# Kernel optimization log

Measured on AMD Instinct MI355X. Metric: run time of the kernel, lower is better.

The kernel has to match this reference:

```python
import jax, jax.numpy as jnp
import numpy as np

VOCAB = 50257
WORD_DIM = 300
HIDDEN = 256
BATCH = 256   # number of trees
LEAVES = 1024  # leaves per complete binary tree (power of 2)


def setup_inputs() -> dict:
    key = jax.random.key(0)
    k_ids, k_emb, k_w1, k_b1, k_w2, k_b2 = jax.random.split(key, 6)
    word_ids = jax.random.randint(k_ids, (BATCH, LEAVES), 0, VOCAB)
    emb_table = jax.random.normal(k_emb, (VOCAB, WORD_DIM), dtype=jnp.float32) * 0.1
    W1 = jax.random.normal(k_w1, (WORD_DIM, HIDDEN), dtype=jnp.float32) * (1.0 / np.sqrt(WORD_DIM))
    b1 = jax.random.normal(k_b1, (HIDDEN,), dtype=jnp.float32) * 0.01
    W2 = jax.random.normal(k_w2, (2 * HIDDEN, HIDDEN), dtype=jnp.float32) * (1.0 / np.sqrt(2 * HIDDEN))
    b2 = jax.random.normal(k_b2, (HIDDEN,), dtype=jnp.float32) * 0.01
    return {"word_ids": word_ids, "emb_table": emb_table, "W1": W1, "b1": b1, "W2": W2, "b2": b2}


def reference(word_ids, emb_table, W1, b1, W2, b2):
    # Leaves: embedding lookup + word2hidden linear (no nonlinearity, as in source)
    h = jnp.einsum('blw,wh->blh', emb_table[word_ids], W1) + b1  # [B, L, H]
    # Internal nodes: concat(left, right) @ W2 + b2, level by level up the
    # complete binary tree. Loop count = log2(LEAVES), a small static constant.
    while h.shape[1] > 1:
        B, n, H = h.shape
        pairs = h.reshape(B, n // 2, 2 * H)  # concat of sibling states
        h = jnp.einsum('bnk,kh->bnh', pairs, W2) + b2
    return h[:, 0, :]  # root hidden state per tree: [B, H]
```

## Files before the change

### kernel.cpp

```cpp
#include <hip/hip_runtime.h>
#include <hip/hip_bf16.h>
#include <stdint.h>

#define VOCAB 50257
#define WD 300
#define KP1 320
#define MP 50432

using bf16 = __hip_bfloat16;
typedef __attribute__((ext_vector_type(4))) float f32x4;
typedef __attribute__((ext_vector_type(8))) short bf16x8;

__device__ __forceinline__ void async_load16(const void* g, void* l) {
    __builtin_amdgcn_global_load_lds(
        (const __attribute__((address_space(1))) uint32_t*)(uintptr_t)g,
        (__attribute__((address_space(3))) uint32_t*)l, 16, 0, 0);
}

__global__ void prep_w(const float* __restrict__ W1, const float* __restrict__ W2,
                       const float* __restrict__ b2,
                       bf16* __restrict__ w1t, bf16* __restrict__ w2t,
                       bf16* __restrict__ w2b, float* __restrict__ b4,
                       float* __restrict__ zbuf) {
    if (blockIdx.x == 1344) {
        __shared__ float b2s[256];
        int n = threadIdx.x;
        b2s[n] = b2[n];
        zbuf[n] = 0.0f;
        __syncthreads();
        float acc = b2s[n];
        #pragma unroll 8
        for (int k = 0; k < 256; ++k)
            acc += b2s[k] * (W2[k * 256 + n] + W2[(k + 256) * 256 + n]);
        b4[n] = acc;
        return;
    }
    int idx = blockIdx.x * 256 + threadIdx.x;
    if (idx < 256 * KP1) {
        int n = idx / KP1;
        int k = idx - n * KP1;
        w1t[idx] = __float2bfloat16(k < WD ? W1[k * 256 + n] : 0.0f);
    } else if (idx < 256 * KP1 + 131072) {
        int j = idx - 256 * KP1;
        int n = j >> 9, k = j & 511;
        w2t[j] = __float2bfloat16(W2[k * 256 + n]);
    } else {
        int j = idx - 256 * KP1 - 131072;
        w2b[j] = __float2bfloat16(W2[j]);
    }
}

template <int AMODE, bool OUT_F32>
__device__ __forceinline__ void tile_gemm(
    char* smem, const void* Av, const int* ids,
    const bf16* BT, int Bstr, const float* bias,
    void* C, int Cs, int coff, int K, int As, int m0,
    const float* zbuf)
{
    constexpr int ASZ = (AMODE == 2) ? 16384 : 8192;
    constexpr int BSZ = 16384, STAGE = ASZ + BSZ;

    const int t = threadIdx.x, w = t >> 6, lane = t & 63;
    const int rg = w >> 2, cgr = w & 3, mi = lane & 15, q = lane >> 4;
    const bf16* Ab = (const bf16*)Av;

    auto stage = [&](int ke, int buf) {
        char* Asm = smem + buf * STAGE;
        char* Bsm = Asm + ASZ;
        if constexpr (AMODE == 2) {
            const float* A32 = (const float*)Av;
            #pragma unroll
            for (int i = 0; i < 2; ++i) {
                int s = i * 512 + t;
                int row = s >> 3;
                int kcd = (s & 7) ^ (row & 7);
                int k = ke + kcd * 4;
                int grow = m0 + row; if (grow >= VOCAB) grow = VOCAB - 1;
                const float* g = (k <= 296) ? (A32 + (size_t)grow * WD + k) : zbuf;
                async_load16(g, Asm + i * 8192 + w * 1024);
            }
        } else {
            int row = t >> 2;
            int kcd = (t & 3) ^ ((row >> 2) & 3);
            const bf16* g = Ab + (size_t)(m0 + row) * As + ke + kcd * 8;
            async_load16(g, Asm + w * 1024);
        }
        #pragma unroll
        for (int i = 0; i < 2; ++i) {
            int s = i * 512 + t;
            int col = s >> 2;
            int kcd = (s & 3) ^ ((col >> 2) & 3);
            async_load16(BT + (size_t)col * Bstr + ke + kcd * 8,
                         Bsm + i * 8192 + w * 1024);
        }
    };

    f32x4 acc[4][4] = {};

    auto compute = [&](int buf) {
        const char* Asm = smem + buf * STAGE;
        const bf16* Bs16 = (const bf16*)(Asm + ASZ);
        bf16x8 af[4], bfr[4];
        if constexpr (AMODE == 2) {
            const float* As32 = (const float*)Asm;
            #pragma unroll
            for (int r = 0; r < 4; ++r) {
                int row = rg * 64 + r * 16 + mi;
                int sl = row * 8 + ((2 * q) ^ (row & 7));
                f32x4 lo = *(const f32x4*)(As32 + sl * 4);
                f32x4 hi = *(const f32x4*)(As32 + (sl ^ 1) * 4);
                union { bf16x8 v; bf16 hh[8]; } u;
                #pragma unroll
                for (int j = 0; j < 4; ++j) u.hh[j] = __float2bfloat16(lo[j]);
                #pragma unroll
                for (int j = 0; j < 4; ++j) u.hh[4 + j] = __float2bfloat16(hi[j]);
                af[r] = u.v;
            }
        } else {
            const bf16* As16 = (const bf16*)Asm;
            #pragma unroll
            for (int r = 0; r < 4; ++r) {
                int row = rg * 64 + r * 16 + mi;
                int slot = row * 4 + (q ^ ((row >> 2) & 3));
                af[r] = *(const bf16x8*)(As16 + slot * 8);
            }
        }
        #pragma unroll
        for (int c = 0; c < 4; ++c) {
            int col = cgr * 64 + c * 16 + mi;
            int slot = col * 4 + (q ^ ((col >> 2) & 3));
            bfr[c] = *(const bf16x8*)(Bs16 + slot * 8);
        }
        #pragma unroll
        for (int r = 0; r < 4; ++r)
            #pragma unroll
            for (int c = 0; c < 4; ++c)
                acc[r][c] = __builtin_amdgcn_mfma_f32_16x16x32_bf16(af[r], bfr[c], acc[r][c], 0, 0, 0);
    };

    const int S = K >> 5;
    if constexpr (AMODE == 2) {
        stage(0, 0);
        for (int k0 = 0; k0 < S; ++k0) {
            if (k0 + 1 < S) {
                stage((k0 + 1) * 32, (k0 + 1) & 1);
                asm volatile("s_waitcnt vmcnt(4)\n\ts_barrier" ::: "memory");
            } else {
                asm volatile("s_waitcnt vmcnt(0)\n\ts_barrier" ::: "memory");
            }
            compute(k0 & 1);
            asm volatile("s_waitcnt lgkmcnt(0)\n\ts_barrier" ::: "memory");
        }
    } else {
        stage(0, 0);
        if (S > 1) stage(32, 1);
        for (int k0 = 0; k0 < S; ++k0) {
            if (k0 + 1 < S)
                asm volatile("s_waitcnt vmcnt(3)\n\ts_barrier" ::: "memory");
            else
                asm volatile("s_waitcnt vmcnt(0)\n\ts_barrier" ::: "memory");
            if (k0 + 2 < S) stage((k0 + 2) * 32, (k0 + 2) % 3);
            compute(k0 % 3);
        }
    }

    #pragma unroll
    for (int r = 0; r < 4; ++r) {
        int rowb = m0 + rg * 64 + r * 16 + q * 4;
        #pragma unroll
        for (int c = 0; c < 4; ++c) {
            int col = cgr * 64 + c * 16 + mi;
            float bv = bias[col];
            #pragma unroll
            for (int i = 0; i < 4; ++i) {
                float v = acc[r][c][i] + bv;
                size_t o = (size_t)(rowb + i) * Cs + coff + col;
                if (OUT_F32) ((float*)C)[o] = v;
                else         ((bf16*)C)[o] = __float2bfloat16(v);
            }
        }
    }
    (void)ids;
}

__global__ __launch_bounds__(512)
void combo(const float* __restrict__ emb, const bf16* __restrict__ w1t,
           const float* __restrict__ b1, const bf16* __restrict__ w2t,
           const bf16* __restrict__ w2b, bf16* __restrict__ w4t,
           bf16* __restrict__ proj, const float* __restrict__ zbuf) {
    __shared__ char smem[73728];
    int blk = blockIdx.x;
    if (blk < 8) {
        int j = blk >> 1, s = blk & 1;
        tile_gemm<0, false>(smem, w2t + 256 * (j >> 1), nullptr,
                            w2b + 65536 * (j & 1), 256, zbuf,
                            w4t, 1024, 256 * j, 256, 512, s * 128, nullptr);
    } else {
        tile_gemm<2, false>(smem, emb, nullptr, w1t, KP1, b1,
                            proj, 256, 0, KP1, WD, (blk - 8) * 128, zbuf);
    }
}

__global__ __launch_bounds__(512)
void w4cK(const bf16* __restrict__ w4t, bf16* __restrict__ w4c) {
    const int tid = blockIdx.x * 512 + threadIdx.x;
    #pragma unroll
    for (int i = 0; i < 8; ++i) {
        int u = i * 4096 + tid;
        int ln = u & 63, ks = (u >> 6) & 31, cg = u >> 11;
        int mi2 = ln & 15, q2 = ln >> 4;
        *(int4*)(w4c + (size_t)u * 8) =
            *(const int4*)(w4t + (size_t)(cg * 16 + mi2) * 1024 + ks * 32 + q2 * 8);
    }
}

__global__ __launch_bounds__(512)
void mainK(const bf16* __restrict__ proj, const int* __restrict__ ids,
           const bf16* __restrict__ w4c, const float* __restrict__ b4,
           bf16* __restrict__ h) {
    __shared__ char Abuf[4][8192];
    const int t = threadIdx.x, w = t >> 6, lane = t & 63;
    const int mi = lane & 15, q = lane >> 4;
    const int rt = blockIdx.x >> 1, ch = blockIdx.x & 1;
    const int m0 = rt * 128;
    const int c0 = ch * 128;
    const int cg = ch * 8 + w;

    const int4 idq = ((const int4*)ids)[m0 + (t >> 2)];

    auto stageA = [&](int r, int buf) {
        int ke = r * 32;
        int row = t >> 2;
        int kcd = (t & 3) ^ ((row >> 2) & 3);
        int sel = ke >> 8;
        int id = (sel & 2) ? ((sel & 1) ? idq.w : idq.z)
                           : ((sel & 1) ? idq.y : idq.x);
        async_load16(proj + (size_t)id * 256 + (ke & 255) + kcd * 8,
                     Abuf[buf] + w * 1024);
        (void)row;
    };

    f32x4 acc[8] = {};
    bf16x8 bp[2];

    stageA(0, 0); stageA(1, 1);
    bp[0] = *(const bf16x8*)(w4c + ((size_t)(cg * 32 + 0) * 64 + lane) * 8);

    #pragma unroll
    for (int r = 0; r < 32; ++r) {
        if (r + 2 < 32) stageA(r + 2, (r + 2) & 3);
        if (r + 1 < 32)
            bp[(r + 1) & 1] = *(const bf16x8*)(
                w4c + ((size_t)(cg * 32 + (r + 1)) * 64 + lane) * 8);
        if (r + 1 < 32)
            asm volatile("s_waitcnt vmcnt(2) lgkmcnt(0)\n\ts_barrier" ::: "memory");
        else
            asm volatile("s_waitcnt vmcnt(0) lgkmcnt(0)\n\ts_barrier" ::: "memory");
        const bf16* As16 = (const bf16*)Abuf[r & 3];
        #pragma unroll
        for (int ri = 0; ri < 8; ++ri) {
            int row = ri * 16 + mi;
            int slot = row * 4 + (q ^ ((row >> 2) & 3));
            bf16x8 af = *(const bf16x8*)(As16 + slot * 8);
            acc[ri] = __builtin_amdgcn_mfma_f32_16x16x32_bf16(af, bp[r & 1], acc[ri], 0, 0, 0);
        }
    }

    const int col = c0 + w * 16 + mi;
    const float bv = b4[col];
    #pragma unroll
    for (int ri = 0; ri < 8; ++ri) {
        int rowb = m0 + ri * 16 + q * 4;
        #pragma unroll
        for (int i = 0; i < 4; ++i)
            h[(size_t)(rowb + i) * 256 + col] = __float2bfloat16(acc[ri][i] + bv);
    }
}

__global__ __launch_bounds__(512)
void treeK(const bf16* __restrict__ h, const bf16* __restrict__ w4t,
           const bf16* __restrict__ w4c, const float* __restrict__ b4,
           float* __restrict__ out) {
    constexpr int ASZ = 8192, BSZ = 32768, STAGE = ASZ + BSZ;
    __shared__ char smem[2 * STAGE];
    __shared__ bf16 Ht[64 * 256];
    __shared__ bf16 Ht2[16 * 256];
    __shared__ bf16 Ht3[4 * 256];

    const int t = threadIdx.x, w = t >> 6, lane = t & 63;
    const int mi = lane & 15, q = lane >> 4;
    const int b = blockIdx.x;

    {
        auto stage = [&](int r, int buf) {
            char* As = smem + buf * STAGE;
            char* Bs = As + ASZ;
            const int kb = r * 64;
            {
                int row = t >> 3, c = t & 7;
                async_load16(h + (size_t)(64 * b + row) * 1024 + kb + ((c ^ (row & 7)) << 3),
                             As + w * 1024);
            }
            #pragma unroll
            for (int sub = 0; sub < 2; ++sub)
                #pragma unroll
                for (int i = 0; i < 2; ++i) {
                    int s = i * 512 + t;
                    int col = s >> 2;
                    int kcd = (s & 3) ^ ((col >> 2) & 3);
                    async_load16(w4t + (size_t)col * 1024 + kb + sub * 32 + kcd * 8,
                                 Bs + sub * 16384 + i * 8192 + w * 1024);
                }
        };
        f32x4 acc[4][2] = {};
        stage(0, 0);
        for (int r = 0; r < 16; ++r) {
            if (r + 1 < 16) {
                stage(r + 1, (r + 1) & 1);
                asm volatile("s_waitcnt vmcnt(5)\n\ts_barrier" ::: "memory");
            } else {
                asm volatile("s_waitcnt vmcnt(0)\n\ts_barrier" ::: "memory");
            }
            const bf16* As16 = (const bf16*)(smem + (r & 1) * STAGE);
            const bf16* Bb   = (const bf16*)(smem + (r & 1) * STAGE + ASZ);
            #pragma unroll
            for (int kk = 0; kk < 2; ++kk) {
                bf16x8 af[4], bfr[2];
                #pragma unroll
                for (int ri = 0; ri < 4; ++ri) {
                    int row = ri * 16 + mi;
                    int c = kk * 4 + q;
                    af[ri] = *(const bf16x8*)(As16 + (row * 8 + (c ^ (row & 7))) * 8);
                }
                #pragma unroll
                for (int c4 = 0; c4 < 2; ++c4) {
                    int col = w * 32 + c4 * 16 + mi;
                    int slot = col * 4 + (q ^ ((col >> 2) & 3));
                    bfr[c4] = *(const bf16x8*)(Bb + kk * 8192 + slot * 8);
                }
                #pragma unroll
                for (int ri = 0; ri < 4; ++ri)
                    #pragma unroll
                    for (int c4 = 0; c4 < 2; ++c4)
                        acc[ri][c4] = __builtin_amdgcn_mfma_f32_16x16x32_bf16(af[ri], bfr[c4], acc[ri][c4], 0, 0, 0);
            }
            asm volatile("s_waitcnt lgkmcnt(0)\n\ts_barrier" ::: "memory");
        }
        #pragma unroll
        for (int ri = 0; ri < 4; ++ri) {
            #pragma unroll
            for (int c4 = 0; c4 < 2; ++c4) {
                int col = w * 32 + c4 * 16 + mi;
                float bv = b4[col];
                int chunk = col >> 3;
                #pragma unroll
                for (int i = 0; i < 4; ++i) {
                    int row = ri * 16 + q * 4 + i;
                    Ht[(row * 32 + (chunk ^ (row & 31))) * 8 + (col & 7)] =
                        __float2bfloat16(acc[ri][c4][i] + bv);
                }
            }
        }
    }
    __syncthreads();

    {
        f32x4 acc[2] = {};
        #pragma unroll 8
        for (int ks = 0; ks < 32; ++ks) {
            int kc = (ks & 7) * 4 + q;
            int r2 = 4 * mi + (ks >> 3);
            bf16x8 a = *(const bf16x8*)(Ht + (r2 * 32 + (kc ^ (r2 & 31))) * 8);
            #pragma unroll
            for (int g = 0; g < 2; ++g) {
                bf16x8 bb = *(const bf16x8*)(w4c + ((size_t)((2 * w + g) * 32 + ks) * 64 + lane) * 8);
                acc[g] = __builtin_amdgcn_mfma_f32_16x16x32_bf16(a, bb, acc[g], 0, 0, 0);
            }
        }
        #pragma unroll
        for (int g = 0; g < 2; ++g) {
            int col = w * 32 + g * 16 + mi;
            float bv = b4[col];
            int chunk = col >> 3;
            #pragma unroll
            for (int i = 0; i < 4; ++i) {
                int row = q * 4 + i;
                Ht2[(row * 32 + (chunk ^ (row & 15))) * 8 + (col & 7)] =
                    __float2bfloat16(acc[g][i] + bv);
            }
        }
    }
    __syncthreads();

    {
        f32x4 acc[2] = {};
        #pragma unroll 8
        for (int ks = 0; ks < 32; ++ks) {
            int kc = (ks & 7) * 4 + q;
            int r3 = (4 * mi + (ks >> 3)) & 15;
            bf16x8 a = *(const bf16x8*)(Ht2 + (r3 * 32 + (kc ^ (r3 & 15))) * 8);
            #pragma unroll
            for (int g = 0; g < 2; ++g) {
                bf16x8 bb = *(const bf16x8*)(w4c + ((size_t)((2 * w + g) * 32 + ks) * 64 + lane) * 8);
                acc[g] = __builtin_amdgcn_mfma_f32_16x16x32_bf16(a, bb, acc[g], 0, 0, 0);
            }
        }
        if (q == 0) {
            #pragma unroll
            for (int g = 0; g < 2; ++g) {
                int col = w * 32 + g * 16 + mi;
                float bv = b4[col];
                #pragma unroll
                for (int i = 0; i < 4; ++i)
                    Ht3[i * 256 + col] = __float2bfloat16(acc[g][i] + bv);
            }
        }
    }
    __syncthreads();

    {
        f32x4 acc[2] = {};
        #pragma unroll 8
        for (int ks = 0; ks < 32; ++ks) {
            int r4 = (4 * mi + (ks >> 3)) & 3;
            bf16x8 a = *(const bf16x8*)(Ht3 + r4 * 256 + (ks & 7) * 32 + q * 8);
            #pragma unroll
            for (int g = 0; g < 2; ++g) {
                bf16x8 bb = *(const bf16x8*)(w4c + ((size_t)((2 * w + g) * 32 + ks) * 64 + lane) * 8);
                acc[g] = __builtin_amdgcn_mfma_f32_16x16x32_bf16(a, bb, acc[g], 0, 0, 0);
            }
        }
        if (q == 0) {
            #pragma unroll
            for (int g = 0; g < 2; ++g) {
                int col = w * 32 + g * 16 + mi;
                out[(size_t)b * 256 + col] = acc[g][0] + b4[col];
            }
        }
    }
}

extern "C" void kernel_launch(void* const* d_in, const int* in_sizes, int n_in,
                              void* d_out, int out_size, void* d_ws, size_t ws_size,
                              hipStream_t stream) {
    const int*   ids = (const int*)d_in[0];
    const float* emb = (const float*)d_in[1];
    const float* W1  = (const float*)d_in[2];
    const float* b1  = (const float*)d_in[3];
    const float* W2  = (const float*)d_in[4];
    const float* b2  = (const float*)d_in[5];
    (void)in_sizes; (void)n_in; (void)out_size; (void)ws_size;

    char* ws = (char*)d_ws;
    size_t off = 0;
    float* zbuf = (float*)(ws + off); off += 1024;
    float* b4   = (float*)(ws + off); off += 1024;
    bf16* w1t = (bf16*)(ws + off); off += (size_t)256 * KP1 * 2;
    bf16* w2t = (bf16*)(ws + off); off += (size_t)256 * 512 * 2;
    bf16* w2b = (bf16*)(ws + off); off += (size_t)512 * 256 * 2;
    bf16* w4t = (bf16*)(ws + off); off += (size_t)256 * 1024 * 2;
    bf16* w4c = (bf16*)(ws + off); off += (size_t)256 * 1024 * 2;
    bf16* proj = (bf16*)(ws + off); off += (size_t)MP * 256 * 2;
    bf16* h  = (bf16*)(ws + off); off += (size_t)65536 * 256 * 2;
    (void)off;

    prep_w<<<1345, 256, 0, stream>>>(W1, W2, b2, w1t, w2t, w2b, b4, zbuf);

    combo<<<402, 512, 0, stream>>>(emb, w1t, b1, w2t, w2b, w4t, proj, zbuf);

    w4cK<<<8, 512, 0, stream>>>(w4t, w4c);

    mainK<<<1024, 512, 0, stream>>>(proj, ids, w4c, b4, h);

    treeK<<<256, 512, 0, stream>>>(h, w4t, w4c, b4, (float*)d_out);
}
```

Baseline: 223.0 us.

## Compute full 256-column output per block with 4x4 register tiles in mainK

mainK now has each block cover all 256 output columns for its 128 rows instead of splitting columns across two blocks, which halves the grid to 512 blocks. Each wave computes a 64x64 tile (4 row fragments by 4 column fragments) so every A fragment read from LDS is reused across four B fragments, and the gathered A rows are loaded only once. The aim is to remove the duplicated A gathers and cut LDS reads per MFMA. In exchange it raises register pressure (16 accumulators plus 8 B fragments) and halves the number of blocks, with wait counts retuned for the larger B prefetch.

```diff
diff --git a/kernel.cpp b/kernel.cpp
--- a/kernel.cpp
+++ b/kernel.cpp
@@ -220,60 +220,83 @@
            bf16* __restrict__ h) {
     __shared__ char Abuf[4][8192];
     const int t = threadIdx.x, w = t >> 6, lane = t & 63;
-    const int mi = lane & 15, q = lane >> 4;
-    const int rt = blockIdx.x >> 1, ch = blockIdx.x & 1;
-    const int m0 = rt * 128;
-    const int c0 = ch * 128;
-    const int cg = ch * 8 + w;
+    const int rg = w >> 2, cgr = w & 3, mi = lane & 15, q = lane >> 4;
+    const int m0 = blockIdx.x * 128;
 
     const int4 idq = ((const int4*)ids)[m0 + (t >> 2)];
 
     auto stageA = [&](int r, int buf) {
         int ke = r * 32;
-        int row = t >> 2;
-        int kcd = (t & 3) ^ ((row >> 2) & 3);
+        int kcd = (t & 3) ^ (((t >> 2) >> 2) & 3);
         int sel = ke >> 8;
         int id = (sel & 2) ? ((sel & 1) ? idq.w : idq.z)
                            : ((sel & 1) ? idq.y : idq.x);
         async_load16(proj + (size_t)id * 256 + (ke & 255) + kcd * 8,
                      Abuf[buf] + w * 1024);
-        (void)row;
-    };
-
-    f32x4 acc[8] = {};
-    bf16x8 bp[2];
+    };
+
+    f32x4 acc[4][4] = {};
+    bf16x8 bp0[4], bp1[4];
+
+    auto loadB0 = [&](int r) {
+        #pragma unroll
+        for (int c = 0; c < 4; ++c)
+            bp0[c] = *(const bf16x8*)(
+                w4c + ((size_t)((cgr * 4 + c) * 32 + r) * 64 + lane) * 8);
+    };
+    auto loadB1 = [&](int r) {
+        #pragma unroll
+        for (int c = 0; c < 4; ++c)
+            bp1[c] = *(const bf16x8*)(
+                w4c + ((size_t)((cgr * 4 + c) * 32 + r) * 64 + lane) * 8);
+    };
+
+    auto doMfma = [&](const bf16* As16, const bf16x8* bp) {
+        bf16x8 af[4];
+        #pragma unroll
+        for (int ri = 0; ri < 4; ++ri) {
+            int row = rg * 64 + ri * 16 + mi;
+            int slot = row * 4 + (q ^ ((row >> 2) & 3));
+            af[ri] = *(const bf16x8*)(As16 + slot * 8);
+        }
+        #pragma unroll
+        for (int ri = 0; ri < 4; ++ri)
+            #pragma unroll
+            for (int c = 0; c < 4; ++c)
+                acc[ri][c] = __builtin_amdgcn_mfma_f32_16x16x32_bf16(
+                    af[ri], bp[c], acc[ri][c], 0, 0, 0);
+    };
 
     stageA(0, 0); stageA(1, 1);
-    bp[0] = *(const bf16x8*)(w4c + ((size_t)(cg * 32 + 0) * 64 + lane) * 8);
+    loadB0(0);
+
+    for (int rr = 0; rr < 30; rr += 2) {
+        stageA(rr + 2, (rr + 2) & 3);
+        loadB1(rr + 1);
+        asm volatile("s_waitcnt vmcnt(10) lgkmcnt(0)\n\ts_barrier" ::: "memory");
+        doMfma((const bf16*)Abuf[rr & 3], bp0);
+        stageA(rr + 3, (rr + 3) & 3);
+        loadB0(rr + 2);
+        asm volatile("s_waitcnt vmcnt(10) lgkmcnt(0)\n\ts_barrier" ::: "memory");
+        doMfma((const bf16*)Abuf[(rr + 1) & 3], bp1);
+    }
+    loadB1(31);
+    asm volatile("s_waitcnt vmcnt(9) lgkmcnt(0)\n\ts_barrier" ::: "memory");
+    doMfma((const bf16*)Abuf[30 & 3], bp0);
+    asm volatile("s_waitcnt vmcnt(0) lgkmcnt(0)\n\ts_barrier" ::: "memory");
+    doMfma((const bf16*)Abuf[31 & 3], bp1);
 
     #pragma unroll
-    for (int r = 0; r < 32; ++r) {
-        if (r + 2 < 32) stageA(r + 2, (r + 2) & 3);
-        if (r + 1 < 32)
-            bp[(r + 1) & 1] = *(const bf16x8*)(
-                w4c + ((size_t)(cg * 32 + (r + 1)) * 64 + lane) * 8);
-        if (r + 1 < 32)
-            asm volatile("s_waitcnt vmcnt(2) lgkmcnt(0)\n\ts_barrier" ::: "memory");
-        else
-            asm volatile("s_waitcnt vmcnt(0) lgkmcnt(0)\n\ts_barrier" ::: "memory");
-        const bf16* As16 = (const bf16*)Abuf[r & 3];
-        #pragma unroll
-        for (int ri = 0; ri < 8; ++ri) {
-            int row = ri * 16 + mi;
-            int slot = row * 4 + (q ^ ((row >> 2) & 3));
-            bf16x8 af = *(const bf16x8*)(As16 + slot * 8);
-            acc[ri] = __builtin_amdgcn_mfma_f32_16x16x32_bf16(af, bp[r & 1], acc[ri], 0, 0, 0);
-        }
-    }
-
-    const int col = c0 + w * 16 + mi;
-    const float bv = b4[col];
-    #pragma unroll
-    for (int ri = 0; ri < 8; ++ri) {
-        int rowb = m0 + ri * 16 + q * 4;
-        #pragma unroll
-        for (int i = 0; i < 4; ++i)
-            h[(size_t)(rowb + i) * 256 + col] = __float2bfloat16(acc[ri][i] + bv);
+    for (int ri = 0; ri < 4; ++ri) {
+        int rowb = m0 + rg * 64 + ri * 16 + q * 4;
+        #pragma unroll
+        for (int c = 0; c < 4; ++c) {
+            int col = cgr * 64 + c * 16 + mi;
+            float bv = b4[col];
+            #pragma unroll
+            for (int i = 0; i < 4; ++i)
+                h[(size_t)(rowb + i) * 256 + col] = __float2bfloat16(acc[ri][c][i] + bv);
+        }
     }
 }
 
@@ -470,7 +493,7 @@
 
     w4cK<<<8, 512, 0, stream>>>(w4t, w4c);
 
-    mainK<<<1024, 512, 0, stream>>>(proj, ids, w4c, b4, h);
+    mainK<<<512, 512, 0, stream>>>(proj, ids, w4c, b4, h);
 
     treeK<<<256, 512, 0, stream>>>(h, w4t, w4c, b4, (float*)d_out);
 }
```

Measured after the change: 213.3 us. 1.05x faster.
